# Optimization experiments

Hardware: AMD Instinct MI355X
Metric: run time of the kernel (lower is better)

## Reference

```python
import jax, jax.numpy as jnp
import numpy as np
import math

N_EMBED = 2048
N_HEAD = 16
HEAD_DIM = N_EMBED // N_HEAD  # 128
ROPE_BASE = 10000.0


def _rope_tables(T, dim, dtype):
    # inv_freq over even indices, emb = concat(freqs, freqs) along last dim
    inv_freq = 1.0 / (ROPE_BASE ** (jnp.arange(0, dim, 2, dtype=jnp.float32) / dim))
    t = jnp.arange(T, dtype=jnp.float32)
    freqs = jnp.einsum('i,j->ij', t, inv_freq)          # [T, dim/2]
    emb = jnp.concatenate([freqs, freqs], axis=-1)      # [T, dim]
    return jnp.cos(emb).astype(dtype), jnp.sin(emb).astype(dtype)


def _rotate_half(x):
    h = x.shape[-1] // 2
    return jnp.concatenate([-x[..., h:], x[..., :h]], axis=-1)


def setup_inputs() -> dict:
    key = jax.random.key(0)
    ks = jax.random.split(key, 5)
    B, T, C = 32, 256, N_EMBED
    s = 1.0 / math.sqrt(C)
    return {
        'x': jax.random.normal(ks[0], (B, T, C), dtype=jnp.float32),
        'wq': jax.random.normal(ks[1], (C, C), dtype=jnp.float32) * s,
        'wk': jax.random.normal(ks[2], (C, C), dtype=jnp.float32) * s,
        'wv': jax.random.normal(ks[3], (C, C), dtype=jnp.float32) * s,
        'wo': jax.random.normal(ks[4], (C, C), dtype=jnp.float32) * s,
    }


def reference(x, wq, wk, wv, wo):
    B, T, C = x.shape
    H, D = N_HEAD, HEAD_DIM
    # torch Linear: y = x @ W^T
    q = (x @ wq.T).reshape(B, T, H, D).transpose(0, 2, 1, 3)  # [B,H,T,D]
    k = (x @ wk.T).reshape(B, T, H, D).transpose(0, 2, 1, 3)
    v = (x @ wv.T).reshape(B, T, H, D).transpose(0, 2, 1, 3)

    cos, sin = _rope_tables(T, D, x.dtype)  # [T,D] each, broadcast over B,H
    q = q * cos + _rotate_half(q) * sin
    k = k * cos + _rotate_half(k) * sin

    att = jnp.einsum('bhqd,bhkd->bhqk', q, k) / math.sqrt(D)
    causal = jnp.triu(jnp.ones((T, T), dtype=bool), k=1)
    att = jnp.where(causal, jnp.finfo(att.dtype).min, att)
    att = jax.nn.softmax(att, axis=-1)
    # dropout p=0.0 -> identity
    y = jnp.einsum('bhqk,bhkd->bhqd', att, v)
    y = y.transpose(0, 2, 1, 3).reshape(B, T, C)
    return y @ wo.T
```

## Files before the change

kernel.cpp:

```cpp
#include <hip/hip_runtime.h>

#define HB 32
#define HT 256
#define HC 2048
#define HH 16
#define HD 128
#define HM (HB * HT)

typedef __bf16 bf16x8 __attribute__((ext_vector_type(8)));
typedef float f32x4 __attribute__((ext_vector_type(4)));

__device__ __forceinline__ unsigned short f2bf(float f) {
  unsigned u = __float_as_uint(f);
  u += 0x7FFFu + ((u >> 16) & 1u);
  return (unsigned short)(u >> 16);
}
__device__ __forceinline__ float bf2f(unsigned short h) {
  return __uint_as_float(((unsigned)h) << 16);
}

__global__ __launch_bounds__(256) void cvt_all(
    const float* __restrict__ x, const float* __restrict__ wq, const float* __restrict__ wk,
    const float* __restrict__ wv, const float* __restrict__ wo,
    unsigned short* __restrict__ xb, unsigned short* __restrict__ wqb,
    unsigned short* __restrict__ wkb, unsigned short* __restrict__ wvb,
    unsigned short* __restrict__ wob) {
  size_t i = (size_t)blockIdx.x * 256 + threadIdx.x;
  const float* src;
  unsigned short* dst;
  size_t off;
  if (i < 4194304) {
    src = x; dst = xb; off = i;
  } else {
    size_t j = i - 4194304;
    int w = (int)(j >> 20);
    off = j & 1048575;
    src = (w == 0) ? wq : (w == 1) ? wk : (w == 2) ? wv : wo;
    dst = (w == 0) ? wqb : (w == 1) ? wkb : (w == 2) ? wvb : wob;
  }
  float4 v = ((const float4*)src)[off];
  ushort4 o;
  o.x = f2bf(v.x); o.y = f2bf(v.y); o.z = f2bf(v.z); o.w = f2bf(v.w);
  ((ushort4*)dst)[off] = o;
}

__device__ __forceinline__ void gl_lds16(const unsigned short* g, unsigned short* l) {
  __builtin_amdgcn_global_load_lds((const __attribute__((address_space(1))) void*)g,
                                   (__attribute__((address_space(3))) void*)l, 16, 0, 0);
}

__device__ __forceinline__ void gemm_core(const unsigned short* __restrict__ Ab,
                                          const unsigned short* __restrict__ Wb,
                                          unsigned short* lsA, unsigned short* lsB,
                                          f32x4 acc[4][4], int tid) {
  const int lane = tid & 63, wave = tid >> 6;
  const int quad = lane >> 4, l16 = lane & 15;
  const int wr = wave >> 1, wc = wave & 1;
  for (int kt = 0; kt < HC / 64; ++kt) {
    __syncthreads();
#pragma unroll
    for (int i = 0; i < 4; i++) {
      int c = i * 256 + tid;
      int row = c >> 3, cc = c & 7;
      int gc = cc ^ (row & 7);
      gl_lds16(Ab + (size_t)row * HC + kt * 64 + gc * 8, lsA + c * 8);
      gl_lds16(Wb + (size_t)row * HC + kt * 64 + gc * 8, lsB + c * 8);
    }
    __syncthreads();
#pragma unroll
    for (int ks = 0; ks < 2; ++ks) {
      bf16x8 af[4], bfr[4];
#pragma unroll
      for (int mi = 0; mi < 4; mi++) {
        int r = wr * 64 + mi * 16 + l16;
        int cc = (ks * 4 + quad) ^ (r & 7);
        af[mi] = *(const bf16x8*)(lsA + r * 64 + cc * 8);
      }
#pragma unroll
      for (int ni = 0; ni < 4; ni++) {
        int r = wc * 64 + ni * 16 + l16;
        int cc = (ks * 4 + quad) ^ (r & 7);
        bfr[ni] = *(const bf16x8*)(lsB + r * 64 + cc * 8);
      }
#pragma unroll
      for (int mi = 0; mi < 4; mi++)
#pragma unroll
        for (int ni = 0; ni < 4; ni++)
          acc[mi][ni] = __builtin_amdgcn_mfma_f32_16x16x32_bf16(af[mi], bfr[ni], acc[mi][ni], 0, 0, 0);
    }
  }
}

__global__ __launch_bounds__(256) void gemm_out(const unsigned short* __restrict__ A,
                                                const unsigned short* __restrict__ W,
                                                float* __restrict__ outp) {
  __shared__ __align__(16) unsigned short lsA[128 * 64];
  __shared__ __align__(16) unsigned short lsB[128 * 64];
  const int tid = threadIdx.x;
  const int lane = tid & 63, wave = tid >> 6;
  const int quad = lane >> 4, l16 = lane & 15;
  const int wr = wave >> 1, wc = wave & 1;
  const int bm = blockIdx.x, bn = blockIdx.y;

  f32x4 acc[4][4];
#pragma unroll
  for (int i = 0; i < 4; i++)
#pragma unroll
    for (int j = 0; j < 4; j++) acc[i][j] = f32x4{0.f, 0.f, 0.f, 0.f};

  gemm_core(A + (size_t)bm * 128 * HC, W + (size_t)bn * 128 * HC, lsA, lsB, acc, tid);

#pragma unroll
  for (int mi = 0; mi < 4; mi++)
#pragma unroll
    for (int ni = 0; ni < 4; ni++)
#pragma unroll
      for (int r = 0; r < 4; r++) {
        int m = bm * 128 + wr * 64 + mi * 16 + quad * 4 + r;
        int n = bn * 128 + wc * 64 + ni * 16 + l16;
        outp[(size_t)m * HC + n] = acc[mi][ni][r];
      }
}

__global__ __launch_bounds__(256) void gemm_qkv(const unsigned short* __restrict__ A,
                                                const unsigned short* __restrict__ W0,
                                                const unsigned short* __restrict__ W1,
                                                const unsigned short* __restrict__ W2,
                                                unsigned short* __restrict__ Qo,
                                                unsigned short* __restrict__ Ko,
                                                unsigned short* __restrict__ Vto) {
  __shared__ __align__(16) unsigned short lsA[128 * 64];
  __shared__ __align__(16) unsigned short lsB[128 * 64];
  const int tid = threadIdx.x;
  const int lane = tid & 63, wave = tid >> 6;
  const int quad = lane >> 4, l16 = lane & 15;
  const int wr = wave >> 1, wc = wave & 1;
  const int bm = blockIdx.x;
  const int which = blockIdx.y >> 4;
  const int bn = blockIdx.y & 15;
  const unsigned short* W = (which == 0) ? W0 : (which == 1) ? W1 : W2;
  unsigned short* outp = (which == 0) ? Qo : (which == 1) ? Ko : Vto;

  f32x4 acc[4][4];
#pragma unroll
  for (int i = 0; i < 4; i++)
#pragma unroll
    for (int j = 0; j < 4; j++) acc[i][j] = f32x4{0.f, 0.f, 0.f, 0.f};

  gemm_core(A + (size_t)bm * 128 * HC, W + (size_t)bn * 128 * HC, lsA, lsB, acc, tid);

#pragma unroll
  for (int mi = 0; mi < 4; mi++)
#pragma unroll
    for (int ni = 0; ni < 4; ni++)
#pragma unroll
      for (int r = 0; r < 4; r++) {
        int m = bm * 128 + wr * 64 + mi * 16 + quad * 4 + r;
        int n = bn * 128 + wc * 64 + ni * 16 + l16;
        unsigned short v = f2bf(acc[mi][ni][r]);
        if (which < 2) {
          size_t idx = ((((size_t)(m >> 8) * HH + (n >> 7)) * HT + (m & 255)) * HD) + (n & 127);
          outp[idx] = v;
        } else {
          size_t idx = ((((size_t)(m >> 8) * HH + (n >> 7)) * HD + (n & 127)) * HT) + (m & 255);
          outp[idx] = v;
        }
      }
}

__global__ __launch_bounds__(256) void rope_kernel(unsigned short* __restrict__ Q,
                                                   unsigned short* __restrict__ K) {
  int idx = blockIdx.x * 256 + threadIdx.x;
  int row = idx >> 4;
  int dq = (idx & 15) * 4;
  int t = row & (HT - 1);
  size_t base = (size_t)row * HD;

  ushort4 q0 = *(const ushort4*)(Q + base + dq);
  ushort4 q1 = *(const ushort4*)(Q + base + 64 + dq);
  ushort4 k0 = *(const ushort4*)(K + base + dq);
  ushort4 k1 = *(const ushort4*)(K + base + 64 + dq);

  float c[4], s[4];
#pragma unroll
  for (int j = 0; j < 4; j++) {
    float ang = (float)t * __expf((float)(dq + j) * (-0.14391156831212787f));
    c[j] = cosf(ang);
    s[j] = sinf(ang);
  }
  unsigned short* q0p = (unsigned short*)&q0;
  unsigned short* q1p = (unsigned short*)&q1;
  unsigned short* k0p = (unsigned short*)&k0;
  unsigned short* k1p = (unsigned short*)&k1;
#pragma unroll
  for (int j = 0; j < 4; j++) {
    float a = bf2f(q0p[j]), b = bf2f(q1p[j]);
    q0p[j] = f2bf(a * c[j] - b * s[j]);
    q1p[j] = f2bf(b * c[j] + a * s[j]);
    float ka = bf2f(k0p[j]), kb = bf2f(k1p[j]);
    k0p[j] = f2bf(ka * c[j] - kb * s[j]);
    k1p[j] = f2bf(kb * c[j] + ka * s[j]);
  }
  *(ushort4*)(Q + base + dq) = q0;
  *(ushort4*)(Q + base + 64 + dq) = q1;
  *(ushort4*)(K + base + dq) = k0;
  *(ushort4*)(K + base + 64 + dq) = k1;
}

__global__ __launch_bounds__(256, 4) void attn_kernel(const unsigned short* __restrict__ Q,
                                                      const unsigned short* __restrict__ K,
                                                      const unsigned short* __restrict__ Vt,
                                                      unsigned short* __restrict__ Y) {
  const int g = blockIdx.x;
  const int wq = 3 - (g >> 9);
  const int bh = g & 511;
  const int wave = threadIdx.x >> 6;
  const int lane = threadIdx.x & 63;
  const int quad = lane >> 4, l16 = lane & 15;

  const unsigned short* Qh = Q + (size_t)bh * HT * HD;
  const unsigned short* Kh = K + (size_t)bh * HT * HD;
  const unsigned short* Vh = Vt + (size_t)bh * HD * HT;

  __shared__ __align__(16) unsigned short P[4][16 * 72];
  unsigned short* Pw = P[wave];

  const int qrow = wq * 64 + wave * 16;

  bf16x8 qf[4];
#pragma unroll
  for (int ks = 0; ks < 4; ks++)
    qf[ks] = *(const bf16x8*)(Qh + (size_t)(qrow + l16) * HD + ks * 32 + quad * 8);

  f32x4 o[8];
#pragma unroll
  for (int di = 0; di < 8; di++) o[di] = f32x4{0.f, 0.f, 0.f, 0.f};
  float mrow[4], lrow[4];
#pragma unroll
  for (int r = 0; r < 4; r++) { mrow[r] = -1e30f; lrow[r] = 0.f; }

  const float scale = 0.088388347648318447f;

  for (int ct = 0; ct <= wq; ++ct) {
    f32x4 s[4];
#pragma unroll
    for (int ni = 0; ni < 4; ni++) s[ni] = f32x4{0.f, 0.f, 0.f, 0.f};
    const int nimax = (ct == wq) ? wave : 3;
#pragma unroll
    for (int ks = 0; ks < 4; ks++) {
#pragma unroll
      for (int ni = 0; ni < 4; ni++) {
        if (ni <= nimax) {
          bf16x8 kf = *(const bf16x8*)(Kh + (size_t)(ct * 64 + ni * 16 + l16) * HD + ks * 32 + quad * 8);
          s[ni] = __builtin_amdgcn_mfma_f32_16x16x32_bf16(qf[ks], kf, s[ni], 0, 0, 0);
        }
      }
    }
    if (ct == wq) {
#pragma unroll
      for (int ni = 0; ni < 4; ni++)
#pragma unroll
        for (int r = 0; r < 4; r++) {
          int qr = wave * 16 + quad * 4 + r;
          int kc = ni * 16 + l16;
          s[ni][r] = (kc <= qr) ? s[ni][r] * scale : -1e30f;
        }
    } else {
#pragma unroll
      for (int ni = 0; ni < 4; ni++)
#pragma unroll
        for (int r = 0; r < 4; r++) s[ni][r] *= scale;
    }
#pragma unroll
    for (int r = 0; r < 4; r++) {
      float v = fmaxf(fmaxf(s[0][r], s[1][r]), fmaxf(s[2][r], s[3][r]));
      v = fmaxf(v, __shfl_xor(v, 1, 64));
      v = fmaxf(v, __shfl_xor(v, 2, 64));
      v = fmaxf(v, __shfl_xor(v, 4, 64));
      v = fmaxf(v, __shfl_xor(v, 8, 64));
      float mnew = fmaxf(mrow[r], v);
      float alpha = __expf(mrow[r] - mnew);
      mrow[r] = mnew;
      float rs = 0.f;
#pragma unroll
      for (int ni = 0; ni < 4; ni++) {
        float e = __expf(s[ni][r] - mnew);
        s[ni][r] = e;
        rs += e;
      }
      rs += __shfl_xor(rs, 1, 64);
      rs += __shfl_xor(rs, 2, 64);
      rs += __shfl_xor(rs, 4, 64);
      rs += __shfl_xor(rs, 8, 64);
      lrow[r] = lrow[r] * alpha + rs;
#pragma unroll
      for (int di = 0; di < 8; di++) o[di][r] *= alpha;
    }
#pragma unroll
    for (int ni = 0; ni < 4; ni++)
#pragma unroll
      for (int r = 0; r < 4; r++)
        Pw[(quad * 4 + r) * 72 + ni * 16 + l16] = f2bf(s[ni][r]);
#pragma unroll
    for (int ks = 0; ks < 2; ks++) {
      bf16x8 pf = *(const bf16x8*)(Pw + (size_t)l16 * 72 + ks * 32 + quad * 8);
#pragma unroll
      for (int di = 0; di < 8; di++) {
        bf16x8 vf = *(const bf16x8*)(Vh + (size_t)(di * 16 + l16) * HT + ct * 64 + ks * 32 + quad * 8);
        o[di] = __builtin_amdgcn_mfma_f32_16x16x32_bf16(pf, vf, o[di], 0, 0, 0);
      }
    }
  }

  const int b = bh >> 4, h = bh & 15;
#pragma unroll
  for (int r = 0; r < 4; r++) {
    float inv = 1.f / lrow[r];
    int t = qrow + quad * 4 + r;
    size_t rowb = ((size_t)b * HT + t) * HC + h * HD;
#pragma unroll
    for (int di = 0; di < 8; di++)
      Y[rowb + di * 16 + l16] = f2bf(o[di][r] * inv);
  }
}

extern "C" void kernel_launch(void* const* d_in, const int* in_sizes, int n_in,
                              void* d_out, int out_size, void* d_ws, size_t ws_size,
                              hipStream_t stream) {
  const float* x  = (const float*)d_in[0];
  const float* wq = (const float*)d_in[1];
  const float* wk = (const float*)d_in[2];
  const float* wv = (const float*)d_in[3];
  const float* wo = (const float*)d_in[4];
  float* out = (float*)d_out;

  char* ws = (char*)d_ws;
  const size_t MB = (size_t)1 << 20;
  unsigned short* wqb = (unsigned short*)(ws + 0 * MB);
  unsigned short* wkb = (unsigned short*)(ws + 8 * MB);
  unsigned short* wvb = (unsigned short*)(ws + 16 * MB);
  unsigned short* wob = (unsigned short*)(ws + 24 * MB);
  unsigned short* xb  = (unsigned short*)(ws + 32 * MB);
  unsigned short* Qb  = (unsigned short*)(ws + 64 * MB);
  unsigned short* Kb  = (unsigned short*)(ws + 96 * MB);
  unsigned short* Vtb = (unsigned short*)(ws + 128 * MB);
  unsigned short* Yb  = xb;

  cvt_all<<<32768, 256, 0, stream>>>(x, wq, wk, wv, wo, xb, wqb, wkb, wvb, wob);

  gemm_qkv<<<dim3(HM / 128, 48), 256, 0, stream>>>(xb, wqb, wkb, wvb, Qb, Kb, Vtb);

  rope_kernel<<<8192, 256, 0, stream>>>(Qb, Kb);

  attn_kernel<<<2048, 256, 0, stream>>>(Qb, Kb, Vtb, Yb);

  gemm_out<<<dim3(HM / 128, HC / 128), 256, 0, stream>>>(Yb, wob, out);
}
```

Measured before the change: 608.1 us.

## Switch GEMMs to 32x32 MFMA, fuse RoPE into QKV epilogue, swap V operands

Replaces the 16x16x32 MFMA tiling with 32x32x16 MFMA in both projection GEMMs, rearranging the N-tile mapping so each lane holds the d and d+64 columns of a head. This pairing lets the RoPE rotation be applied in the Q/K GEMM epilogue, removing the separate rope kernel and its read/write pass over Q and K. For V, the operands are swapped so the transposed Vt layout is written with lane-contiguous t indices for better coalescing. The trade-off is extra sincos work in the epilogue and a different register layout for the accumulators.

```diff
diff --git a/kernel.cpp b/kernel.cpp
--- a/kernel.cpp
+++ b/kernel.cpp
@@ -9,6 +9,7 @@
 
 typedef __bf16 bf16x8 __attribute__((ext_vector_type(8)));
 typedef float f32x4 __attribute__((ext_vector_type(4)));
+typedef float f32x16 __attribute__((ext_vector_type(16)));
 
 __device__ __forceinline__ unsigned short f2bf(float f) {
   unsigned u = __float_as_uint(f);
@@ -49,12 +50,12 @@
                                    (__attribute__((address_space(3))) void*)l, 16, 0, 0);
 }
 
-__device__ __forceinline__ void gemm_core(const unsigned short* __restrict__ Ab,
-                                          const unsigned short* __restrict__ Wb,
-                                          unsigned short* lsA, unsigned short* lsB,
-                                          f32x4 acc[4][4], int tid) {
+__device__ __forceinline__ void gemm_core32(const unsigned short* __restrict__ Ab,
+                                            const unsigned short* __restrict__ Wb,
+                                            unsigned short* lsA, unsigned short* lsB,
+                                            f32x16 acc[2][2], int tid) {
   const int lane = tid & 63, wave = tid >> 6;
-  const int quad = lane >> 4, l16 = lane & 15;
+  const int l31 = lane & 31, half = lane >> 5;
   const int wr = wave >> 1, wc = wave & 1;
   for (int kt = 0; kt < HC / 64; ++kt) {
     __syncthreads();
@@ -68,25 +69,26 @@
     }
     __syncthreads();
 #pragma unroll
-    for (int ks = 0; ks < 2; ++ks) {
-      bf16x8 af[4], bfr[4];
-#pragma unroll
-      for (int mi = 0; mi < 4; mi++) {
-        int r = wr * 64 + mi * 16 + l16;
-        int cc = (ks * 4 + quad) ^ (r & 7);
+    for (int ks = 0; ks < 4; ++ks) {
+      const int g = ks * 2 + half;
+      bf16x8 af[2], bfr[2];
+#pragma unroll
+      for (int mi = 0; mi < 2; mi++) {
+        int r = wr * 64 + mi * 32 + l31;
+        int cc = g ^ (r & 7);
         af[mi] = *(const bf16x8*)(lsA + r * 64 + cc * 8);
       }
 #pragma unroll
-      for (int ni = 0; ni < 4; ni++) {
-        int r = wc * 64 + ni * 16 + l16;
-        int cc = (ks * 4 + quad) ^ (r & 7);
-        bfr[ni] = *(const bf16x8*)(lsB + r * 64 + cc * 8);
-      }
-#pragma unroll
-      for (int mi = 0; mi < 4; mi++)
-#pragma unroll
-        for (int ni = 0; ni < 4; ni++)
-          acc[mi][ni] = __builtin_amdgcn_mfma_f32_16x16x32_bf16(af[mi], bfr[ni], acc[mi][ni], 0, 0, 0);
+      for (int nj = 0; nj < 2; nj++) {
+        int r = nj * 64 + wc * 32 + l31;
+        int cc = g ^ (r & 7);
+        bfr[nj] = *(const bf16x8*)(lsB + r * 64 + cc * 8);
+      }
+#pragma unroll
+      for (int mi = 0; mi < 2; mi++)
+#pragma unroll
+        for (int nj = 0; nj < 2; nj++)
+          acc[mi][nj] = __builtin_amdgcn_mfma_f32_32x32x16_bf16(af[mi], bfr[nj], acc[mi][nj], 0, 0, 0);
     }
   }
 }
@@ -98,28 +100,32 @@
   __shared__ __align__(16) unsigned short lsB[128 * 64];
   const int tid = threadIdx.x;
   const int lane = tid & 63, wave = tid >> 6;
-  const int quad = lane >> 4, l16 = lane & 15;
+  const int l31 = lane & 31, half = lane >> 5;
   const int wr = wave >> 1, wc = wave & 1;
   const int bm = blockIdx.x, bn = blockIdx.y;
 
-  f32x4 acc[4][4];
-#pragma unroll
-  for (int i = 0; i < 4; i++)
-#pragma unroll
-    for (int j = 0; j < 4; j++) acc[i][j] = f32x4{0.f, 0.f, 0.f, 0.f};
-
-  gemm_core(A + (size_t)bm * 128 * HC, W + (size_t)bn * 128 * HC, lsA, lsB, acc, tid);
-
-#pragma unroll
-  for (int mi = 0; mi < 4; mi++)
-#pragma unroll
-    for (int ni = 0; ni < 4; ni++)
-#pragma unroll
-      for (int r = 0; r < 4; r++) {
-        int m = bm * 128 + wr * 64 + mi * 16 + quad * 4 + r;
-        int n = bn * 128 + wc * 64 + ni * 16 + l16;
-        outp[(size_t)m * HC + n] = acc[mi][ni][r];
-      }
+  f32x16 acc[2][2];
+#pragma unroll
+  for (int i = 0; i < 2; i++)
+#pragma unroll
+    for (int j = 0; j < 2; j++)
+#pragma unroll
+      for (int r = 0; r < 16; r++) acc[i][j][r] = 0.f;
+
+  gemm_core32(A + (size_t)bm * 128 * HC, W + (size_t)bn * 128 * HC, lsA, lsB, acc, tid);
+
+#pragma unroll
+  for (int mi = 0; mi < 2; mi++)
+#pragma unroll
+    for (int nj = 0; nj < 2; nj++)
+#pragma unroll
+      for (int g = 0; g < 4; g++)
+#pragma unroll
+        for (int rr = 0; rr < 4; rr++) {
+          int m = bm * 128 + wr * 64 + mi * 32 + rr + 8 * g + 4 * half;
+          int n = bn * 128 + nj * 64 + wc * 32 + l31;
+          outp[(size_t)m * HC + n] = acc[mi][nj][g * 4 + rr];
+        }
 }
 
 __global__ __launch_bounds__(256) void gemm_qkv(const unsigned short* __restrict__ A,
@@ -133,78 +139,61 @@
   __shared__ __align__(16) unsigned short lsB[128 * 64];
   const int tid = threadIdx.x;
   const int lane = tid & 63, wave = tid >> 6;
-  const int quad = lane >> 4, l16 = lane & 15;
+  const int l31 = lane & 31, half = lane >> 5;
   const int wr = wave >> 1, wc = wave & 1;
   const int bm = blockIdx.x;
   const int which = blockIdx.y >> 4;
   const int bn = blockIdx.y & 15;
-  const unsigned short* W = (which == 0) ? W0 : (which == 1) ? W1 : W2;
-  unsigned short* outp = (which == 0) ? Qo : (which == 1) ? Ko : Vto;
-
-  f32x4 acc[4][4];
-#pragma unroll
-  for (int i = 0; i < 4; i++)
-#pragma unroll
-    for (int j = 0; j < 4; j++) acc[i][j] = f32x4{0.f, 0.f, 0.f, 0.f};
-
-  gemm_core(A + (size_t)bm * 128 * HC, W + (size_t)bn * 128 * HC, lsA, lsB, acc, tid);
-
-#pragma unroll
-  for (int mi = 0; mi < 4; mi++)
-#pragma unroll
-    for (int ni = 0; ni < 4; ni++)
-#pragma unroll
-      for (int r = 0; r < 4; r++) {
-        int m = bm * 128 + wr * 64 + mi * 16 + quad * 4 + r;
-        int n = bn * 128 + wc * 64 + ni * 16 + l16;
-        unsigned short v = f2bf(acc[mi][ni][r]);
-        if (which < 2) {
-          size_t idx = ((((size_t)(m >> 8) * HH + (n >> 7)) * HT + (m & 255)) * HD) + (n & 127);
-          outp[idx] = v;
-        } else {
-          size_t idx = ((((size_t)(m >> 8) * HH + (n >> 7)) * HD + (n & 127)) * HT) + (m & 255);
-          outp[idx] = v;
+
+  f32x16 acc[2][2];
+#pragma unroll
+  for (int i = 0; i < 2; i++)
+#pragma unroll
+    for (int j = 0; j < 2; j++)
+#pragma unroll
+      for (int r = 0; r < 16; r++) acc[i][j][r] = 0.f;
+
+  if (which < 2) {
+    const unsigned short* W = (which == 0) ? W0 : W1;
+    unsigned short* outp = (which == 0) ? Qo : Ko;
+    gemm_core32(A + (size_t)bm * 128 * HC, W + (size_t)bn * 128 * HC, lsA, lsB, acc, tid);
+    const int dlo = wc * 32 + l31;
+    const float invf = __expf((float)dlo * (-0.14391156831212787f));
+    const int h = bn;
+#pragma unroll
+    for (int mi = 0; mi < 2; mi++)
+#pragma unroll
+      for (int g = 0; g < 4; g++)
+#pragma unroll
+        for (int rr = 0; rr < 4; rr++) {
+          int m = bm * 128 + wr * 64 + mi * 32 + rr + 8 * g + 4 * half;
+          int t = m & 255, b = m >> 8;
+          float ang = (float)t * invf;
+          float sn, cs;
+          __sincosf(ang, &sn, &cs);
+          int reg = g * 4 + rr;
+          float lo = acc[mi][0][reg], hi = acc[mi][1][reg];
+          size_t base = (((size_t)b * HH + h) * HT + t) * HD;
+          outp[base + dlo] = f2bf(lo * cs - hi * sn);
+          outp[base + 64 + dlo] = f2bf(hi * cs + lo * sn);
         }
-      }
-}
-
-__global__ __launch_bounds__(256) void rope_kernel(unsigned short* __restrict__ Q,
-                                                   unsigned short* __restrict__ K) {
-  int idx = blockIdx.x * 256 + threadIdx.x;
-  int row = idx >> 4;
-  int dq = (idx & 15) * 4;
-  int t = row & (HT - 1);
-  size_t base = (size_t)row * HD;
-
-  ushort4 q0 = *(const ushort4*)(Q + base + dq);
-  ushort4 q1 = *(const ushort4*)(Q + base + 64 + dq);
-  ushort4 k0 = *(const ushort4*)(K + base + dq);
-  ushort4 k1 = *(const ushort4*)(K + base + 64 + dq);
-
-  float c[4], s[4];
-#pragma unroll
-  for (int j = 0; j < 4; j++) {
-    float ang = (float)t * __expf((float)(dq + j) * (-0.14391156831212787f));
-    c[j] = cosf(ang);
-    s[j] = sinf(ang);
-  }
-  unsigned short* q0p = (unsigned short*)&q0;
-  unsigned short* q1p = (unsigned short*)&q1;
-  unsigned short* k0p = (unsigned short*)&k0;
-  unsigned short* k1p = (unsigned short*)&k1;
-#pragma unroll
-  for (int j = 0; j < 4; j++) {
-    float a = bf2f(q0p[j]), b = bf2f(q1p[j]);
-    q0p[j] = f2bf(a * c[j] - b * s[j]);
-    q1p[j] = f2bf(b * c[j] + a * s[j]);
-    float ka = bf2f(k0p[j]), kb = bf2f(k1p[j]);
-    k0p[j] = f2bf(ka * c[j] - kb * s[j]);
-    k1p[j] = f2bf(kb * c[j] + ka * s[j]);
-  }
-  *(ushort4*)(Q + base + dq) = q0;
-  *(ushort4*)(Q + base + 64 + dq) = q1;
-  *(ushort4*)(K + base + dq) = k0;
-  *(ushort4*)(K + base + 64 + dq) = k1;
+  } else {
+    gemm_core32(W2 + (size_t)bn * 128 * HC, A + (size_t)bm * 128 * HC, lsA, lsB, acc, tid);
+    const int h = bn;
+#pragma unroll
+    for (int mi = 0; mi < 2; mi++)
+#pragma unroll
+      for (int nj = 0; nj < 2; nj++)
+#pragma unroll
+        for (int g = 0; g < 4; g++)
+#pragma unroll
+          for (int rr = 0; rr < 4; rr++) {
+            int d = wr * 64 + mi * 32 + rr + 8 * g + 4 * half;
+            int np = bm * 128 + nj * 64 + wc * 32 + l31;
+            int b = np >> 8, t = np & 255;
+            Vto[(((size_t)b * HH + h) * HD + d) * HT + t] = f2bf(acc[mi][nj][g * 4 + rr]);
+          }
+  }
 }
 
 __global__ __launch_bounds__(256, 4) void attn_kernel(const unsigned short* __restrict__ Q,
@@ -350,8 +339,6 @@
 
   gemm_qkv<<<dim3(HM / 128, 48), 256, 0, stream>>>(xb, wqb, wkb, wvb, Qb, Kb, Vtb);
 
-  rope_kernel<<<8192, 256, 0, stream>>>(Qb, Kb);
-
   attn_kernel<<<2048, 256, 0, stream>>>(Qb, Kb, Vtb, Yb);
 
   gemm_out<<<dim3(HM / 128, HC / 128), 256, 0, stream>>>(Yb, wob, out);
```

After: 537.0 us. 1.13x faster.
